# Performance work log

Measured on AMD Instinct MI355X. Metric: run time of the kernel, lower is better.

## Reference

```python
import jax, jax.numpy as jnp
import numpy as np

N_BRANCH, N_LAYER = 4, 3
B, T, D_IN = 4, 1024, 32
D_MODEL, D_INNER, D_STATE, D_CONV, DT_RANK = 128, 256, 16, 4, 8
EMBED = 64
MAX_NORM = 10.0  # safe_expmap0 tangent-norm clip
EPS = 1e-7


def setup_inputs() -> dict:
    key = jax.random.key(0)
    ks = jax.random.split(key, 12)
    def nrm(k, shp, s=0.02):
        return s * jax.random.normal(k, shp, dtype=jnp.float32)
    A_init = jnp.log(jnp.arange(1, D_STATE + 1, dtype=jnp.float32))
    return {
        "trend": jax.random.normal(ks[0], (B, T, D_IN), jnp.float32),
        "seasonal_coarse": jax.random.normal(ks[1], (B, T, D_IN), jnp.float32),
        "seasonal_fine": jax.random.normal(ks[2], (B, T, D_IN), jnp.float32),
        "residual": jax.random.normal(ks[3], (B, T, D_IN), jnp.float32),
        "W_ip": nrm(ks[4], (N_BRANCH, D_IN, D_MODEL)),
        "b_ip": jnp.zeros((N_BRANCH, D_MODEL), jnp.float32),
        "W_in": nrm(ks[5], (N_BRANCH, N_LAYER, D_MODEL, 2 * D_INNER)),
        "conv_w": nrm(ks[6], (N_BRANCH, N_LAYER, D_INNER, D_CONV), 0.1),
        "conv_b": jnp.zeros((N_BRANCH, N_LAYER, D_INNER), jnp.float32),
        "W_x": nrm(ks[7], (N_BRANCH, N_LAYER, D_INNER, DT_RANK + 2 * D_STATE)),
        "W_dt": nrm(ks[8], (N_BRANCH, N_LAYER, DT_RANK, D_INNER), 0.1),
        "b_dt": jnp.full((N_BRANCH, N_LAYER, D_INNER), -4.6, jnp.float32),  # softplus ~ 0.01
        "A_log": jnp.broadcast_to(A_init, (N_BRANCH, N_LAYER, D_INNER, D_STATE)),
        "D_param": jnp.ones((N_BRANCH, N_LAYER, D_INNER), jnp.float32),
        "W_out": nrm(ks[9], (N_BRANCH, N_LAYER, D_INNER, D_MODEL)),
        "W_op": nrm(ks[10], (N_BRANCH, D_MODEL, EMBED)),
        "b_op": jnp.zeros((N_BRANCH, EMBED), jnp.float32),
        "eff_scale": jnp.asarray(0.1, jnp.float32),
    }


def _mamba_layer(x, Win, cw, cb, Wx, Wdt, bdt, Alog, Dp, Wout):
    # x: [B, T, d_model]
    Tlen = x.shape[1]
    xz = x @ Win                                   # [B,T,2*di]
    xp, z = jnp.split(xz, 2, axis=-1)
    # causal depthwise conv1d, kernel D_CONV
    xpad = jnp.pad(xp, ((0, 0), (D_CONV - 1, 0), (0, 0)))
    xc = sum(xpad[:, k:k + Tlen, :] * cw[:, k] for k in range(D_CONV))
    xc = jax.nn.silu(xc + cb)                      # [B,T,di]
    dbl = xc @ Wx                                  # [B,T,r+2s]
    dt = jax.nn.softplus(dbl[..., :DT_RANK] @ Wdt + bdt)   # [B,T,di]
    Bm = dbl[..., DT_RANK:DT_RANK + D_STATE]       # [B,T,s]
    Cm = dbl[..., DT_RANK + D_STATE:]              # [B,T,s]
    A = -jnp.exp(Alog)                             # [di,s]
    dA = jnp.exp(dt[..., None] * A)                # [B,T,di,s]
    dBx = (dt * xc)[..., None] * Bm[:, :, None, :] # [B,T,di,s]

    def step(h, inp):
        dA_t, dBx_t, C_t = inp
        h = dA_t * h + dBx_t
        return h, jnp.einsum('bds,bs->bd', h, C_t)

    h0 = jnp.zeros((x.shape[0], D_INNER, D_STATE), x.dtype)
    _, ys = jax.lax.scan(step, h0, (jnp.swapaxes(dA, 0, 1),
                                     jnp.swapaxes(dBx, 0, 1),
                                     jnp.swapaxes(Cm, 0, 1)))
    y = jnp.swapaxes(ys, 0, 1) + Dp * xc
    return (y * jax.nn.silu(z)) @ Wout


def _embed(x, Wip, bip, Wins, cws, cbs, Wxs, Wdts, bdts, Alogs, Dps, Wouts, Wop, bop):
    h = x @ Wip + bip
    for l in range(N_LAYER):
        h = _mamba_layer(h, Wins[l], cws[l], cbs[l], Wxs[l], Wdts[l], bdts[l],
                         Alogs[l], Dps[l], Wouts[l])
    return h.mean(axis=1) @ Wop + bop              # [B, EMBED]


def _expmap0(v):
    # safe expmap0 on Lorentz (k=1): clip tangent norm at MAX_NORM
    n = jnp.linalg.norm(v, axis=-1, keepdims=True)
    nc = jnp.clip(n, EPS, MAX_NORM)
    v = v * (nc / jnp.maximum(n, EPS))
    return jnp.concatenate([jnp.cosh(nc), jnp.sinh(nc) / nc * v], axis=-1)


def _projx(x):
    sp = x[..., 1:]
    t = jnp.sqrt(1.0 + jnp.sum(sp * sp, axis=-1, keepdims=True))
    return jnp.concatenate([t, sp], axis=-1)


def _logmap0(x):
    sp = x[..., 1:]
    t = jnp.maximum(x[..., :1], 1.0 + EPS)
    d = jnp.arccosh(t)
    spn = jnp.maximum(jnp.linalg.norm(sp, axis=-1, keepdims=True), EPS)
    return d * sp / spn


def _forward(trend, seasonal_coarse, seasonal_fine, residual,
             W_ip, b_ip, W_in, conv_w, conv_b, W_x, W_dt, b_dt,
             A_log, D_param, W_out, W_op, b_op, eff_scale):
    xs = [trend, seasonal_coarse, seasonal_fine, residual]
    z_t = [
        _embed(xs[b], W_ip[b], b_ip[b], W_in[b], conv_w[b], conv_b[b], W_x[b],
               W_dt[b], b_dt[b], A_log[b], D_param[b], W_out[b], W_op[b], b_op[b])
        for b in range(N_BRANCH)
    ]
    es = jnp.tanh(eff_scale)
    z_h = [_projx(_expmap0(z * es)) for z in z_t]
    us = [_logmap0(zh) for zh in z_h]
    combined_tangent = us[0] + us[1] + us[2] + us[3]
    combined_h = _projx(_expmap0(combined_tangent * es))
    return (*z_t, *z_h, combined_tangent, combined_h)


def reference(trend, seasonal_coarse, seasonal_fine, residual,
              W_ip, b_ip, W_in, conv_w, conv_b, W_x, W_dt, b_dt,
              A_log, D_param, W_out, W_op, b_op, eff_scale):
    return _forward(trend, seasonal_coarse, seasonal_fine, residual,
                    W_ip, b_ip, W_in, conv_w, conv_b, W_x, W_dt, b_dt,
                    A_log, D_param, W_out, W_op, b_op, eff_scale)
```

## Files before the change

kernel.cpp:

```cpp
#include <hip/hip_runtime.h>
#include <math.h>

#define NBR 4
#define NLAY 3
#define Bk 4
#define Tk 1024
#define DIN 32
#define DMODEL 128
#define DINNER 256
#define DSTATE 16
#define DTRANK 8
#define EMBEDk 64
#define BT (Bk*Tk)
#define EPSF 1e-7f
#define MAXNF 10.0f
#define LCH 64
#define NCH (Tk/LCH)
#define UF 8
#define NWB 320

typedef __bf16 bf16x8 __attribute__((ext_vector_type(8)));
typedef float  f32x4  __attribute__((ext_vector_type(4)));
typedef unsigned short u16x8 __attribute__((ext_vector_type(8)));

__device__ __forceinline__ float siluf(float x){ return x / (1.f + __expf(-x)); }
__device__ __forceinline__ float softplusf(float x){ return (x > 20.f) ? x : log1pf(__expf(x)); }
__device__ __forceinline__ unsigned short f2b(float x){
    union { float f; unsigned u; } v; v.f = x;
    unsigned r = v.u + 0x7FFF + ((v.u >> 16) & 1);
    return (unsigned short)(r >> 16);
}
__device__ __forceinline__ float b2f(unsigned short u){
    union { unsigned u; float f; } v; v.u = ((unsigned)u) << 16; return v.f;
}

__device__ __forceinline__ void dA_pow(float q, float* dA){
    dA[0] = q;             dA[1] = q * q;
    dA[2] = dA[1] * dA[0]; dA[3] = dA[1] * dA[1];
    dA[4] = dA[3] * dA[0]; dA[5] = dA[3] * dA[1];
    dA[6] = dA[3] * dA[2]; dA[7] = dA[3] * dA[3];
    #pragma unroll
    for (int s = 8; s < 16; ++s) dA[s] = dA[s - 8] * dA[7];
}
__device__ __forceinline__ void dA_exp(float dtv, const float* Aa, float* dA){
    #pragma unroll
    for (int s = 0; s < 16; ++s) dA[s] = __expf(dtv * Aa[s]);
}

template<int MODE>
__global__ __launch_bounds__(256) void bgemm_k(
    const unsigned short* __restrict__ Ab, long aBr, int K,
    const unsigned short* __restrict__ Bt, long bBr,
    float* __restrict__ C0, long c0Br,
    float* __restrict__ C1, long c1Br,
    unsigned short* __restrict__ Cb, long cbBr,
    unsigned short* __restrict__ Cb2, long cb2Br,
    float* __restrict__ Mb,
    const float* __restrict__ bias, long biasBr)
{
    const int br = blockIdx.z;
    Ab += (long)br * aBr;
    Bt += (long)br * bBr;
    if (MODE == 3) { C0 += (long)br * c0Br; C1 += (long)br * c1Br;
                     bias += (long)br * biasBr; }
    if (MODE == 0) { Cb += (long)br * cbBr; Cb2 += (long)br * cb2Br; }
    if (MODE == 1) { Mb += (long)br * (Bk * DMODEL); }
    const int m0 = blockIdx.x * 64, n0 = blockIdx.y * 64;
    __shared__ __align__(16) unsigned short As[8 * 64 * 8];
    __shared__ __align__(16) unsigned short Bs[8 * 64 * 8];
    const int tid = threadIdx.x;
    const int lane = tid & 63, w = tid >> 6;
    const int wm = w >> 1, wn = w & 1;
    const int quad = lane >> 4, l15 = lane & 15;
    f32x4 acc00 = {0,0,0,0}, acc01 = {0,0,0,0}, acc10 = {0,0,0,0}, acc11 = {0,0,0,0};
    for (int kc = 0; kc < K; kc += 64) {
        #pragma unroll
        for (int it = 0; it < 2; ++it) {
            const int c = tid + it * 256;
            const int r = c & 63, kch = c >> 6;
            *(u16x8*)&As[(kch * 64 + r) * 8] =
                *(const u16x8*)(Ab + (long)(m0 + r) * K + kc + kch * 8);
            *(u16x8*)&Bs[(kch * 64 + r) * 8] =
                *(const u16x8*)(Bt + (long)(n0 + r) * K + kc + kch * 8);
        }
        __syncthreads();
        #pragma unroll
        for (int k0 = 0; k0 < 64; k0 += 32) {
            const int kch = (k0 >> 3) + quad;
            bf16x8 a0 = *(const bf16x8*)&As[(kch * 64 + wm * 32 +      l15) * 8];
            bf16x8 a1 = *(const bf16x8*)&As[(kch * 64 + wm * 32 + 16 + l15) * 8];
            bf16x8 b0 = *(const bf16x8*)&Bs[(kch * 64 + wn * 32 +      l15) * 8];
            bf16x8 b1 = *(const bf16x8*)&Bs[(kch * 64 + wn * 32 + 16 + l15) * 8];
            acc00 = __builtin_amdgcn_mfma_f32_16x16x32_bf16(a0, b0, acc00, 0, 0, 0);
            acc01 = __builtin_amdgcn_mfma_f32_16x16x32_bf16(a0, b1, acc01, 0, 0, 0);
            acc10 = __builtin_amdgcn_mfma_f32_16x16x32_bf16(a1, b0, acc10, 0, 0, 0);
            acc11 = __builtin_amdgcn_mfma_f32_16x16x32_bf16(a1, b1, acc11, 0, 0, 0);
        }
        __syncthreads();
    }
    if (MODE == 1) {
        float s0 = 0.f, s1 = 0.f;
        #pragma unroll
        for (int r = 0; r < 4; ++r) { s0 += acc00[r] + acc10[r];
                                      s1 += acc01[r] + acc11[r]; }
        const int bidx = m0 >> 10;
        atomicAdd(&Mb[bidx * DMODEL + n0 + wn * 32 + l15], s0);
        atomicAdd(&Mb[bidx * DMODEL + n0 + wn * 32 + 16 + l15], s1);
        return;
    }
    #pragma unroll
    for (int e = 0; e < 4; ++e) {
        f32x4 a = (e == 0) ? acc00 : (e == 1) ? acc01 : (e == 2) ? acc10 : acc11;
        const int msub = (e >> 1) * 16, nsub = (e & 1) * 16;
        const int col = n0 + wn * 32 + nsub + l15;
        #pragma unroll
        for (int r = 0; r < 4; ++r) {
            const int row = m0 + wm * 32 + msub + quad * 4 + r;
            const float v = a[r];
            if (MODE == 0) {
                if (n0 < 256) Cb[(long)row * 256 + col] = f2b(v);
                else          Cb2[(long)row * 256 + (col - 256)] = f2b(siluf(v));
            } else {
                if (col < 256)      C0[(long)row * 256 + col] = softplusf(v + bias[col]);
                else if (col < 288) C1[(long)row * 32 + (col - 256)] = v;
            }
        }
    }
}

__global__ __launch_bounds__(256) void sgemmW_k(
    const float* __restrict__ Wout, const float* __restrict__ Win,
    float* __restrict__ Wtmp, unsigned* __restrict__ zbuf)
{
    if (blockIdx.x == 0 && blockIdx.y == 0 && blockIdx.z == 0) {
        for (int i = threadIdx.x; i < 4096; i += 256) zbuf[i] = 0u;
    }
    const int z = blockIdx.z, p = z >> 2, br = z & 3;
    const float* A  = Wout + (long)(br * NLAY + p) * DINNER * DMODEL;
    const float* Bw = Win  + (long)(br * NLAY + p + 1) * DMODEL * 512;
    float* C = Wtmp + (long)z * DINNER * 512;
    const int m0 = blockIdx.x * 64, n0 = blockIdx.y * 64;
    __shared__ float As[32][68];
    __shared__ float Bs[32][68];
    const int tid = threadIdx.x;
    const int tx = tid & 15, ty = tid >> 4;
    float acc[4][4] = {};
    for (int kc = 0; kc < DMODEL; kc += 32) {
        #pragma unroll
        for (int it = 0; it < 2; ++it) {
            int id = tid + it * 256;
            int r = id >> 3, c4 = (id & 7) << 2;
            float4 v = *(const float4*)(A + (long)(m0 + r) * DMODEL + kc + c4);
            As[c4+0][r] = v.x; As[c4+1][r] = v.y; As[c4+2][r] = v.z; As[c4+3][r] = v.w;
            int rb = id >> 4, cb = (id & 15) << 2;
            *(float4*)&Bs[rb][cb] = *(const float4*)(Bw + (long)(kc + rb) * 512 + n0 + cb);
        }
        __syncthreads();
        #pragma unroll
        for (int kk = 0; kk < 32; ++kk) {
            float4 a4 = *(const float4*)&As[kk][ty << 2];
            float4 b4 = *(const float4*)&Bs[kk][tx << 2];
            float av[4] = {a4.x, a4.y, a4.z, a4.w};
            float bv[4] = {b4.x, b4.y, b4.z, b4.w};
            #pragma unroll
            for (int i = 0; i < 4; ++i)
                #pragma unroll
                for (int j = 0; j < 4; ++j)
                    acc[i][j] = fmaf(av[i], bv[j], acc[i][j]);
        }
        __syncthreads();
    }
    #pragma unroll
    for (int i = 0; i < 4; ++i) {
        int row = m0 + (ty << 2) + i, col = n0 + (tx << 2);
        float4 v4; v4.x = acc[i][0]; v4.y = acc[i][1]; v4.z = acc[i][2]; v4.w = acc[i][3];
        *(float4*)(C + (long)row * 512 + col) = v4;
    }
}

__device__ void transposeTile(const float* __restrict__ W,
                              unsigned short* __restrict__ o,
                              int Kd, int Nd, int n0, int k0, float* smem)
{
    float (*tile)[65] = (float(*)[65])smem;
    const int t = threadIdx.x;
    #pragma unroll
    for (int i = 0; i < 16; ++i) {
        int idx = t + i * 256;
        int kl = idx >> 6, nl = idx & 63;
        tile[kl][nl] = W[(long)(k0 + kl) * Nd + n0 + nl];
    }
    __syncthreads();
    #pragma unroll
    for (int i = 0; i < 16; ++i) {
        int idx = t + i * 256;
        int nl = idx >> 6, kl = idx & 63;
        o[(long)(n0 + nl) * Kd + k0 + kl] = f2b(tile[kl][nl]);
    }
}

__global__ __launch_bounds__(256) void prepAll_k(
    const float* __restrict__ W_in, const float* __restrict__ Wtmp,
    const float* __restrict__ W_out,
    const float* __restrict__ W_x, const float* __restrict__ W_dt,
    const float* __restrict__ X0, const float* __restrict__ X1,
    const float* __restrict__ X2, const float* __restrict__ X3,
    const float* __restrict__ W_ip, const float* __restrict__ b_ip,
    unsigned short* __restrict__ Win0T, unsigned short* __restrict__ WfT,
    unsigned short* __restrict__ Wo2T, unsigned short* __restrict__ WcT,
    unsigned short* __restrict__ h_bf)
{
    __shared__ float smem[32 * 68 * 2];
    const int id = blockIdx.x;
    if (id < 64) {
        int br = id >> 4, rem = id & 15;
        int nt = rem & 7, kt = rem >> 3;
        transposeTile(W_in + (long)br * NLAY * DMODEL * 512,
                      Win0T + (long)br * 512 * DMODEL,
                      DMODEL, 512, nt * 64, kt * 64, smem);
    } else if (id < 320) {
        int id2 = id - 64;
        int z = id2 >> 5, rem = id2 & 31;
        int nt = rem & 7, kt = rem >> 3;
        transposeTile(Wtmp + (long)z * DINNER * 512,
                      WfT + (long)z * 512 * DINNER,
                      DINNER, 512, nt * 64, kt * 64, smem);
    } else if (id < 352) {
        int id3 = id - 320;
        int br = id3 >> 3, rem = id3 & 7;
        int nt = rem & 1, kt = rem >> 1;
        transposeTile(W_out + ((long)br * NLAY + 2) * DINNER * DMODEL,
                      Wo2T + (long)br * DMODEL * DINNER,
                      DINNER, DMODEL, nt * 64, kt * 64, smem);
    } else if (id < 4192) {
        int id4 = id - 352;
        int bl = id4 / NWB, n = id4 % NWB;
        const int k = threadIdx.x;
        const float* WxP = W_x + (long)bl * DINNER * 40;
        float v;
        if (n < 256) {
            const float* WdtP = W_dt + (long)bl * DTRANK * DINNER;
            float s = 0.f;
            #pragma unroll
            for (int r = 0; r < 8; ++r)
                s = fmaf(WxP[k * 40 + r], WdtP[r * DINNER + n], s);
            v = s;
        } else if (n < 288) {
            v = WxP[k * 40 + 8 + (n - 256)];
        } else {
            v = 0.f;
        }
        WcT[(long)bl * NWB * DINNER + (long)n * DINNER + k] = f2b(v);
    } else {
        int id5 = id - 4192;
        int br = id5 >> 7, rem = id5 & 127;
        int m0 = (rem & 63) * 64, n0 = (rem >> 6) * 64;
        const float* A = (br == 1) ? X1 : (br == 2) ? X2 : (br == 3) ? X3 : X0;
        const float* Bw = W_ip + (long)br * DIN * DMODEL;
        const float* bias = b_ip + (long)br * DMODEL;
        unsigned short* Cb = h_bf + (long)br * BT * DMODEL;
        float (*As)[68] = (float(*)[68])smem;
        float (*Bs)[68] = (float(*)[68])(smem + 32 * 68);
        const int tid = threadIdx.x;
        const int tx = tid & 15, ty = tid >> 4;
        float acc[4][4] = {};
        #pragma unroll
        for (int it = 0; it < 2; ++it) {
            int idd = tid + it * 256;
            int r = idd >> 3, c4 = (idd & 7) << 2;
            float4 v = *(const float4*)(A + (long)(m0 + r) * DIN + c4);
            As[c4+0][r] = v.x; As[c4+1][r] = v.y; As[c4+2][r] = v.z; As[c4+3][r] = v.w;
            int rb = idd >> 4, cb = (idd & 15) << 2;
            *(float4*)&Bs[rb][cb] = *(const float4*)(Bw + (long)rb * DMODEL + n0 + cb);
        }
        __syncthreads();
        #pragma unroll
        for (int kk = 0; kk < 32; ++kk) {
            float4 a4 = *(const float4*)&As[kk][ty << 2];
            float4 b4 = *(const float4*)&Bs[kk][tx << 2];
            float av[4] = {a4.x, a4.y, a4.z, a4.w};
            float bv[4] = {b4.x, b4.y, b4.z, b4.w};
            #pragma unroll
            for (int i = 0; i < 4; ++i)
                #pragma unroll
                for (int j = 0; j < 4; ++j)
                    acc[i][j] = fmaf(av[i], bv[j], acc[i][j]);
        }
        const int col = n0 + (tx << 2);
        #pragma unroll
        for (int i = 0; i < 4; ++i) {
            const int row = m0 + (ty << 2) + i;
            #pragma unroll
            for (int j = 0; j < 4; ++j)
                Cb[(long)row * DMODEL + col + j] = f2b(acc[i][j] + bias[col + j]);
        }
    }
}

__global__ __launch_bounds__(256) void conv_k(
    const unsigned short* __restrict__ xp, const float* __restrict__ cw,
    const float* __restrict__ cb, unsigned short* __restrict__ xcb, int layer)
{
    const int br = blockIdx.y;
    const long base = (long)br * BT * DINNER;
    const int idx = blockIdx.x * 256 + threadIdx.x;
    const int d = idx & (DINNER - 1);
    const int row = idx >> 8;
    const int t = row & (Tk - 1);
    const float4 w4 = *(const float4*)(cw + ((long)(br * NLAY + layer) * DINNER + d) * 4);
    const float wv[4] = {w4.x, w4.y, w4.z, w4.w};
    float acc = cb[(br * NLAY + layer) * DINNER + d];
    const unsigned short* xpb = xp + base + idx;
    #pragma unroll
    for (int k = 0; k < 4; ++k) {
        int tt = t + k - 3;
        if (tt >= 0) acc = fmaf(b2f(xpb[(long)(k - 3) * DINNER]), wv[k], acc);
    }
    xcb[base + idx] = f2b(siluf(acc));
}

__global__ __launch_bounds__(256) void scan1_k(
    const float* __restrict__ dtb, const unsigned short* __restrict__ xcb,
    const float* __restrict__ bcb, const float* __restrict__ Alog,
    float* __restrict__ recbuf, int layer)
{
    const int c = blockIdx.x, b = blockIdx.y, br = blockIdx.z;
    const int d = threadIdx.x;
    const float* Ap = Alog + ((long)(br * NLAY + layer) * DINNER + d) * DSTATE;
    float Aa[16];
    bool pw = true;
    #pragma unroll
    for (int s = 0; s < 16; ++s) {
        Aa[s] = -__expf(Ap[s]);
        pw = pw && (fabsf(Aa[s] + (float)(s + 1)) < 1e-3f);
    }
    const long rbase = (long)br * BT + (long)b * Tk + (long)c * LCH;
    const float* dtp = dtb + rbase * DINNER + d;
    const unsigned short* xcp = xcb + rbase * DINNER + d;
    __shared__ float bcs[LCH * 32];
    {
        const float4* g = (const float4*)(bcb + rbase * 32);
        float4* l = (float4*)bcs;
        l[d] = g[d]; l[d + 256] = g[d + 256];
    }
    float dtc[UF], xcc[UF];
    #pragma unroll
    for (int u = 0; u < UF; ++u) {
        dtc[u] = dtp[(long)u * DINNER];
        xcc[u] = b2f(xcp[(long)u * DINNER]);
    }
    __syncthreads();
    float h[16];
    #pragma unroll
    for (int s = 0; s < 16; ++s) h[s] = 0.f;
    float sumdt = 0.f;
    for (int base = 0; base < LCH; base += UF) {
        const int nb = (base + UF < LCH) ? base + UF : base;
        float dtn[UF], xcn[UF];
        #pragma unroll
        for (int u = 0; u < UF; ++u) {
            dtn[u] = dtp[(long)(nb + u) * DINNER];
            xcn[u] = b2f(xcp[(long)(nb + u) * DINNER]);
        }
        #pragma unroll
        for (int u = 0; u < UF; ++u) {
            const int t = base + u;
            const float dtv = dtc[u];
            const float dtxc = dtv * xcc[u];
            sumdt += dtv;
            float dA[16];
            if (pw) dA_pow(__expf(-dtv), dA);
            else    dA_exp(dtv, Aa, dA);
            const float* bcT = bcs + t * 32;
            #pragma unroll
            for (int s = 0; s < 16; ++s)
                h[s] = fmaf(dA[s], h[s], dtxc * bcT[s]);
        }
        #pragma unroll
        for (int u = 0; u < UF; ++u) { dtc[u] = dtn[u]; xcc[u] = xcn[u]; }
    }
    float* sb = recbuf + (((long)(br * 4 + b) * (NCH - 1) + c) * 17) * 256 + d;
    #pragma unroll
    for (int s = 0; s < 16; ++s) sb[s * 256] = h[s];
    sb[16 * 256] = sumdt;
}

__global__ __launch_bounds__(256) void scan3_k(
    const float* __restrict__ dtb, const unsigned short* __restrict__ xcb,
    const float* __restrict__ bcb, const unsigned short* __restrict__ zb,
    const float* __restrict__ Alog, const float* __restrict__ Dpar,
    const float* __restrict__ recbuf, unsigned short* __restrict__ yzb, int layer)
{
    const int c = blockIdx.x, b = blockIdx.y, br = blockIdx.z;
    const int d = threadIdx.x;
    const float* Ap = Alog + ((long)(br * NLAY + layer) * DINNER + d) * DSTATE;
    float Aa[16];
    bool pw = true;
    #pragma unroll
    for (int s = 0; s < 16; ++s) {
        Aa[s] = -__expf(Ap[s]);
        pw = pw && (fabsf(Aa[s] + (float)(s + 1)) < 1e-3f);
    }
    float h[16];
    #pragma unroll
    for (int s = 0; s < 16; ++s) h[s] = 0.f;
    if (c > 0) {
        const float* recB = recbuf + ((long)(br * 4 + b) * (NCH - 1)) * 17 * 256 + d;
        float rh[16], rs;
        #pragma unroll
        for (int s = 0; s < 16; ++s) rh[s] = recB[s * 256];
        rs = recB[16 * 256];
        for (int cc = 0; cc < c; ++cc) {
            float nh[16], ns = 0.f;
            if (cc + 1 < c) {
                const float* r2 = recB + (long)(cc + 1) * 17 * 256;
                #pragma unroll
                for (int s = 0; s < 16; ++s) nh[s] = r2[s * 256];
                ns = r2[16 * 256];
            } else {
                #pragma unroll
                for (int s = 0; s < 16; ++s) nh[s] = 0.f;
            }
            float P[16];
            if (pw) dA_pow(__expf(-rs), P);
            else    dA_exp(rs, Aa, P);
            #pragma unroll
            for (int s = 0; s < 16; ++s) h[s] = fmaf(h[s], P[s], rh[s]);
            #pragma unroll
            for (int s = 0; s < 16; ++s) rh[s] = nh[s];
            rs = ns;
        }
    }
    const float Dp = Dpar[(br * NLAY + layer) * DINNER + d];
    const long rbase = (long)br * BT + (long)b * Tk + (long)c * LCH;
    const float* dtp = dtb + rbase * DINNER + d;
    const unsigned short* xcp = xcb + rbase * DINNER + d;
    const unsigned short* zp  = zb  + rbase * DINNER + d;
    unsigned short* yp = yzb + rbase * DINNER + d;
    __shared__ float bcs[LCH * 32];
    {
        const float4* g = (const float4*)(bcb + rbase * 32);
        float4* l = (float4*)bcs;
        l[d] = g[d]; l[d + 256] = g[d + 256];
    }
    float dtc[UF], xcc[UF], zc[UF];
    #pragma unroll
    for (int u = 0; u < UF; ++u) {
        dtc[u] = dtp[(long)u * DINNER];
        xcc[u] = b2f(xcp[(long)u * DINNER]);
        zc[u]  = b2f(zp[(long)u * DINNER]);
    }
    __syncthreads();
    for (int base = 0; base < LCH; base += UF) {
        const int nb = (base + UF < LCH) ? base + UF : base;
        float dtn[UF], xcn[UF], zn[UF];
        #pragma unroll
        for (int u = 0; u < UF; ++u) {
            dtn[u] = dtp[(long)(nb + u) * DINNER];
            xcn[u] = b2f(xcp[(long)(nb + u) * DINNER]);
            zn[u]  = b2f(zp[(long)(nb + u) * DINNER]);
        }
        #pragma unroll
        for (int u = 0; u < UF; ++u) {
            const int t = base + u;
            const float dtv = dtc[u], xcv = xcc[u];
            const float dtxc = dtv * xcv;
            float dA[16];
            if (pw) dA_pow(__expf(-dtv), dA);
            else    dA_exp(dtv, Aa, dA);
            const float* bcT = bcs + t * 32;
            #pragma unroll
            for (int s = 0; s < 16; ++s)
                h[s] = fmaf(dA[s], h[s], dtxc * bcT[s]);
            float y0 = 0.f, y1 = 0.f, y2 = 0.f, y3 = 0.f;
            #pragma unroll
            for (int s = 0; s < 16; s += 4) {
                y0 = fmaf(h[s+0], bcT[16+s+0], y0);
                y1 = fmaf(h[s+1], bcT[16+s+1], y1);
                y2 = fmaf(h[s+2], bcT[16+s+2], y2);
                y3 = fmaf(h[s+3], bcT[16+s+3], y3);
            }
            const float y = (y0 + y1) + (y2 + y3) + Dp * xcv;
            yp[(long)t * DINNER] = f2b(y * zc[u]);
        }
        #pragma unroll
        for (int u = 0; u < UF; ++u) { dtc[u] = dtn[u]; xcc[u] = xcn[u]; zc[u] = zn[u]; }
    }
}

__global__ __launch_bounds__(64) void final_k(
    const float* __restrict__ Mb, const float* __restrict__ Wop,
    const float* __restrict__ bop, float* __restrict__ out,
    const float* __restrict__ eff)
{
    __shared__ float hm[NBR * Bk * DMODEL];
    __shared__ float zts[NBR * Bk * EMBEDk];
    __shared__ float us[NBR][Bk][EMBEDk];
    const int t = threadIdx.x;
    for (int i = t; i < NBR * Bk * DMODEL; i += 64) hm[i] = Mb[i] * (1.0f / Tk);
    __syncthreads();
    for (int br = 0; br < NBR; ++br) {
        const float* wp = Wop + (long)br * DMODEL * EMBEDk + t;
        const float bb = bop[br * EMBEDk + t];
        for (int b = 0; b < Bk; ++b) {
            const float* hmp = &hm[(br * Bk + b) * DMODEL];
            float acc = bb;
            for (int k = 0; k < DMODEL; ++k) acc = fmaf(hmp[k], wp[k * EMBEDk], acc);
            out[(br * Bk + b) * EMBEDk + t] = acc;
            zts[(br * Bk + b) * EMBEDk + t] = acc;
        }
    }
    __syncthreads();
    const float es = tanhf(eff[0]);
    if (t < 16) {
        const int br = t >> 2, b = t & 3;
        const float* z = &zts[(br * Bk + b) * EMBEDk];
        float n2 = 0.f;
        for (int e = 0; e < EMBEDk; ++e) { float v = z[e] * es; n2 = fmaf(v, v, n2); }
        const float n  = sqrtf(n2);
        const float nc = fminf(fmaxf(n, EPSF), MAXNF);
        const float sc = nc / fmaxf(n, EPSF);
        const float sh = sinhf(nc) / nc;
        const float fac = es * sc * sh;
        float* zh = out + 1024 + br * (Bk * (EMBEDk + 1)) + b * (EMBEDk + 1);
        float sp2 = 0.f;
        for (int e = 0; e < EMBEDk; ++e) {
            float spv = z[e] * fac;
            sp2 = fmaf(spv, spv, sp2);
            zh[1 + e] = spv;
            us[br][b][e] = spv;
        }
        const float t0 = sqrtf(1.f + sp2);
        zh[0] = t0;
        const float dd  = acoshf(fmaxf(t0, 1.f + EPSF));
        const float spn = fmaxf(sqrtf(sp2), EPSF);
        const float rr  = dd / spn;
        for (int e = 0; e < EMBEDk; ++e) us[br][b][e] *= rr;
    }
    __syncthreads();
    if (t < 4) {
        const int b = t;
        float ct[EMBEDk];
        float* cto = out + 2064 + b * EMBEDk;
        for (int e = 0; e < EMBEDk; ++e) {
            float v = us[0][b][e] + us[1][b][e] + us[2][b][e] + us[3][b][e];
            ct[e] = v; cto[e] = v;
        }
        float n2 = 0.f;
        for (int e = 0; e < EMBEDk; ++e) { float v = ct[e] * es; n2 = fmaf(v, v, n2); }
        const float n  = sqrtf(n2);
        const float nc = fminf(fmaxf(n, EPSF), MAXNF);
        const float sc = nc / fmaxf(n, EPSF);
        const float sh = sinhf(nc) / nc;
        const float fac = es * sc * sh;
        float* ch = out + 2320 + b * (EMBEDk + 1);
        float sp2 = 0.f;
        for (int e = 0; e < EMBEDk; ++e) {
            float spv = ct[e] * fac;
            sp2 = fmaf(spv, spv, sp2);
            ch[1 + e] = spv;
        }
        ch[0] = sqrtf(1.f + sp2);
    }
}

extern "C" void kernel_launch(void* const* d_in, const int* in_sizes, int n_in,
                              void* d_out, int out_size, void* d_ws, size_t ws_size,
                              hipStream_t stream)
{
    const float* X0 = (const float*)d_in[0];
    const float* X1 = (const float*)d_in[1];
    const float* X2 = (const float*)d_in[2];
    const float* X3 = (const float*)d_in[3];
    const float* W_ip   = (const float*)d_in[4];
    const float* b_ip   = (const float*)d_in[5];
    const float* W_in   = (const float*)d_in[6];
    const float* conv_w = (const float*)d_in[7];
    const float* conv_b = (const float*)d_in[8];
    const float* W_x    = (const float*)d_in[9];
    const float* W_dt   = (const float*)d_in[10];
    const float* b_dt   = (const float*)d_in[11];
    const float* A_log  = (const float*)d_in[12];
    const float* D_par  = (const float*)d_in[13];
    const float* W_out  = (const float*)d_in[14];
    const float* W_op   = (const float*)d_in[15];
    const float* b_op   = (const float*)d_in[16];
    const float* eff    = (const float*)d_in[17];
    float* out = (float*)d_out;
    float* ws  = (float*)d_ws;

    float* meanb  = ws + 1024;
    float* buf_dt = ws + 4096;
    float* buf_bc = buf_dt + (long)NBR * BT * DINNER;
    float* recbuf = buf_bc + (long)NBR * BT * 32;
    float* Wtmp   = recbuf + (long)16 * (NCH - 1) * 17 * 256;
    unsigned short* h_bf  = (unsigned short*)(Wtmp + (long)8 * DINNER * 512);
    unsigned short* xp_bf = h_bf  + (long)NBR * BT * DMODEL;
    unsigned short* z_bf  = xp_bf + (long)NBR * BT * DINNER;
    unsigned short* xc_bf = z_bf  + (long)NBR * BT * DINNER;
    unsigned short* yz_bf = xc_bf + (long)NBR * BT * DINNER;
    unsigned short* Win0T = yz_bf + (long)NBR * BT * DINNER;
    unsigned short* WfT   = Win0T + (long)NBR * 512 * DMODEL;
    unsigned short* Wo2T  = WfT   + (long)8 * 512 * DINNER;
    unsigned short* WcT   = Wo2T  + (long)NBR * DMODEL * DINNER;

    sgemmW_k<<<dim3(4, 8, 8), 256, 0, stream>>>(W_out, W_in, Wtmp, (unsigned*)ws);
    prepAll_k<<<4704, 256, 0, stream>>>(
        W_in, Wtmp, W_out, W_x, W_dt, X0, X1, X2, X3, W_ip, b_ip,
        Win0T, WfT, Wo2T, WcT, h_bf);

    for (int l = 0; l < NLAY; ++l) {
        if (l == 0) {
            bgemm_k<0><<<dim3(BT / 64, 8, NBR), 256, 0, stream>>>(
                h_bf, (long)BT * DMODEL, DMODEL, Win0T, (long)512 * DMODEL,
                nullptr, 0, nullptr, 0,
                xp_bf, (long)BT * DINNER, z_bf, (long)BT * DINNER,
                nullptr, nullptr, 0);
        } else {
            bgemm_k<0><<<dim3(BT / 64, 8, NBR), 256, 0, stream>>>(
                yz_bf, (long)BT * DINNER, DINNER,
                WfT + (long)(l - 1) * 4 * 512 * DINNER, (long)512 * DINNER,
                nullptr, 0, nullptr, 0,
                xp_bf, (long)BT * DINNER, z_bf, (long)BT * DINNER,
                nullptr, nullptr, 0);
        }
        conv_k<<<dim3((BT * DINNER) / 256, NBR), 256, 0, stream>>>(
            xp_bf, conv_w, conv_b, xc_bf, l);
        bgemm_k<3><<<dim3(BT / 64, NWB / 64, NBR), 256, 0, stream>>>(
            xc_bf, (long)BT * DINNER, DINNER,
            WcT + (long)l * NWB * DINNER, (long)NLAY * NWB * DINNER,
            buf_dt, (long)BT * DINNER, buf_bc, (long)BT * 32,
            nullptr, 0, nullptr, 0,
            nullptr, b_dt + l * DINNER, (long)NLAY * DINNER);
        scan1_k<<<dim3(NCH - 1, Bk, NBR), 256, 0, stream>>>(
            buf_dt, xc_bf, buf_bc, A_log, recbuf, l);
        scan3_k<<<dim3(NCH, Bk, NBR), 256, 0, stream>>>(
            buf_dt, xc_bf, buf_bc, z_bf, A_log, D_par, recbuf, yz_bf, l);
        if (l == NLAY - 1) {
            bgemm_k<1><<<dim3(BT / 64, DMODEL / 64, NBR), 256, 0, stream>>>(
                yz_bf, (long)BT * DINNER, DINNER,
                Wo2T, (long)DMODEL * DINNER,
                nullptr, 0, nullptr, 0, nullptr, 0, nullptr, 0,
                meanb, nullptr, 0);
        }
    }

    final_k<<<1, 64, 0, stream>>>(meanb, W_op, b_op, out, eff);
}
```

Before: 477.3 us.

## Store dt in bf16, halve scan chunks, widen GEMM K tile, fuse weight prep

```diff
diff --git a/kernel.cpp b/kernel.cpp
--- a/kernel.cpp
+++ b/kernel.cpp
@@ -14,7 +14,7 @@
 #define BT (Bk*Tk)
 #define EPSF 1e-7f
 #define MAXNF 10.0f
-#define LCH 64
+#define LCH 32
 #define NCH (Tk/LCH)
 #define UF 8
 #define NWB 320
@@ -22,6 +22,7 @@
 typedef __bf16 bf16x8 __attribute__((ext_vector_type(8)));
 typedef float  f32x4  __attribute__((ext_vector_type(4)));
 typedef unsigned short u16x8 __attribute__((ext_vector_type(8)));
+typedef unsigned short u16x4 __attribute__((ext_vector_type(4)));
 
 __device__ __forceinline__ float siluf(float x){ return x / (1.f + __expf(-x)); }
 __device__ __forceinline__ float softplusf(float x){ return (x > 20.f) ? x : log1pf(__expf(x)); }
@@ -51,7 +52,6 @@
 __global__ __launch_bounds__(256) void bgemm_k(
     const unsigned short* __restrict__ Ab, long aBr, int K,
     const unsigned short* __restrict__ Bt, long bBr,
-    float* __restrict__ C0, long c0Br,
     float* __restrict__ C1, long c1Br,
     unsigned short* __restrict__ Cb, long cbBr,
     unsigned short* __restrict__ Cb2, long cb2Br,
@@ -61,21 +61,21 @@
     const int br = blockIdx.z;
     Ab += (long)br * aBr;
     Bt += (long)br * bBr;
-    if (MODE == 3) { C0 += (long)br * c0Br; C1 += (long)br * c1Br;
+    if (MODE == 0) { Cb += (long)br * cbBr; Cb2 += (long)br * cb2Br; }
+    if (MODE == 3) { Cb += (long)br * cbBr; C1 += (long)br * c1Br;
                      bias += (long)br * biasBr; }
-    if (MODE == 0) { Cb += (long)br * cbBr; Cb2 += (long)br * cb2Br; }
     if (MODE == 1) { Mb += (long)br * (Bk * DMODEL); }
     const int m0 = blockIdx.x * 64, n0 = blockIdx.y * 64;
-    __shared__ __align__(16) unsigned short As[8 * 64 * 8];
-    __shared__ __align__(16) unsigned short Bs[8 * 64 * 8];
+    __shared__ __align__(16) unsigned short As[16 * 64 * 8];
+    __shared__ __align__(16) unsigned short Bs[16 * 64 * 8];
     const int tid = threadIdx.x;
     const int lane = tid & 63, w = tid >> 6;
     const int wm = w >> 1, wn = w & 1;
     const int quad = lane >> 4, l15 = lane & 15;
     f32x4 acc00 = {0,0,0,0}, acc01 = {0,0,0,0}, acc10 = {0,0,0,0}, acc11 = {0,0,0,0};
-    for (int kc = 0; kc < K; kc += 64) {
-        #pragma unroll
-        for (int it = 0; it < 2; ++it) {
+    for (int kc = 0; kc < K; kc += 128) {
+        #pragma unroll
+        for (int it = 0; it < 4; ++it) {
             const int c = tid + it * 256;
             const int r = c & 63, kch = c >> 6;
             *(u16x8*)&As[(kch * 64 + r) * 8] =
@@ -85,7 +85,7 @@
         }
         __syncthreads();
         #pragma unroll
-        for (int k0 = 0; k0 < 64; k0 += 32) {
+        for (int k0 = 0; k0 < 128; k0 += 32) {
             const int kch = (k0 >> 3) + quad;
             bf16x8 a0 = *(const bf16x8*)&As[(kch * 64 + wm * 32 +      l15) * 8];
             bf16x8 a1 = *(const bf16x8*)&As[(kch * 64 + wm * 32 + 16 + l15) * 8];
@@ -121,60 +121,10 @@
                 if (n0 < 256) Cb[(long)row * 256 + col] = f2b(v);
                 else          Cb2[(long)row * 256 + (col - 256)] = f2b(siluf(v));
             } else {
-                if (col < 256)      C0[(long)row * 256 + col] = softplusf(v + bias[col]);
+                if (col < 256)      Cb[(long)row * 256 + col] = f2b(softplusf(v + bias[col]));
                 else if (col < 288) C1[(long)row * 32 + (col - 256)] = v;
             }
         }
-    }
-}
-
-__global__ __launch_bounds__(256) void sgemmW_k(
-    const float* __restrict__ Wout, const float* __restrict__ Win,
-    float* __restrict__ Wtmp, unsigned* __restrict__ zbuf)
-{
-    if (blockIdx.x == 0 && blockIdx.y == 0 && blockIdx.z == 0) {
-        for (int i = threadIdx.x; i < 4096; i += 256) zbuf[i] = 0u;
-    }
-    const int z = blockIdx.z, p = z >> 2, br = z & 3;
-    const float* A  = Wout + (long)(br * NLAY + p) * DINNER * DMODEL;
-    const float* Bw = Win  + (long)(br * NLAY + p + 1) * DMODEL * 512;
-    float* C = Wtmp + (long)z * DINNER * 512;
-    const int m0 = blockIdx.x * 64, n0 = blockIdx.y * 64;
-    __shared__ float As[32][68];
-    __shared__ float Bs[32][68];
-    const int tid = threadIdx.x;
-    const int tx = tid & 15, ty = tid >> 4;
-    float acc[4][4] = {};
-    for (int kc = 0; kc < DMODEL; kc += 32) {
-        #pragma unroll
-        for (int it = 0; it < 2; ++it) {
-            int id = tid + it * 256;
-            int r = id >> 3, c4 = (id & 7) << 2;
-            float4 v = *(const float4*)(A + (long)(m0 + r) * DMODEL + kc + c4);
-            As[c4+0][r] = v.x; As[c4+1][r] = v.y; As[c4+2][r] = v.z; As[c4+3][r] = v.w;
-            int rb = id >> 4, cb = (id & 15) << 2;
-            *(float4*)&Bs[rb][cb] = *(const float4*)(Bw + (long)(kc + rb) * 512 + n0 + cb);
-        }
-        __syncthreads();
-        #pragma unroll
-        for (int kk = 0; kk < 32; ++kk) {
-            float4 a4 = *(const float4*)&As[kk][ty << 2];
-            float4 b4 = *(const float4*)&Bs[kk][tx << 2];
-            float av[4] = {a4.x, a4.y, a4.z, a4.w};
-            float bv[4] = {b4.x, b4.y, b4.z, b4.w};
-            #pragma unroll
-            for (int i = 0; i < 4; ++i)
-                #pragma unroll
-                for (int j = 0; j < 4; ++j)
-                    acc[i][j] = fmaf(av[i], bv[j], acc[i][j]);
-        }
-        __syncthreads();
-    }
-    #pragma unroll
-    for (int i = 0; i < 4; ++i) {
-        int row = m0 + (ty << 2) + i, col = n0 + (tx << 2);
-        float4 v4; v4.x = acc[i][0]; v4.y = acc[i][1]; v4.z = acc[i][2]; v4.w = acc[i][3];
-        *(float4*)(C + (long)row * 512 + col) = v4;
     }
 }
 
@@ -199,16 +149,15 @@
     }
 }
 
-__global__ __launch_bounds__(256) void prepAll_k(
-    const float* __restrict__ W_in, const float* __restrict__ Wtmp,
-    const float* __restrict__ W_out,
+__global__ __launch_bounds__(256) void prep_k(
+    const float* __restrict__ W_in, const float* __restrict__ W_out,
     const float* __restrict__ W_x, const float* __restrict__ W_dt,
     const float* __restrict__ X0, const float* __restrict__ X1,
     const float* __restrict__ X2, const float* __restrict__ X3,
     const float* __restrict__ W_ip, const float* __restrict__ b_ip,
-    unsigned short* __restrict__ Win0T, unsigned short* __restrict__ WfT,
-    unsigned short* __restrict__ Wo2T, unsigned short* __restrict__ WcT,
-    unsigned short* __restrict__ h_bf)
+    unsigned short* __restrict__ Win0T, unsigned short* __restrict__ Wo2T,
+    unsigned short* __restrict__ WcT, unsigned short* __restrict__ h_bf,
+    unsigned short* __restrict__ WfT, unsigned* __restrict__ zbuf)
 {
     __shared__ float smem[32 * 68 * 2];
     const int id = blockIdx.x;
@@ -218,22 +167,15 @@
         transposeTile(W_in + (long)br * NLAY * DMODEL * 512,
                       Win0T + (long)br * 512 * DMODEL,
                       DMODEL, 512, nt * 64, kt * 64, smem);
-    } else if (id < 320) {
-        int id2 = id - 64;
-        int z = id2 >> 5, rem = id2 & 31;
-        int nt = rem & 7, kt = rem >> 3;
-        transposeTile(Wtmp + (long)z * DINNER * 512,
-                      WfT + (long)z * 512 * DINNER,
-                      DINNER, 512, nt * 64, kt * 64, smem);
-    } else if (id < 352) {
-        int id3 = id - 320;
+    } else if (id < 96) {
+        int id3 = id - 64;
         int br = id3 >> 3, rem = id3 & 7;
         int nt = rem & 1, kt = rem >> 1;
         transposeTile(W_out + ((long)br * NLAY + 2) * DINNER * DMODEL,
                       Wo2T + (long)br * DMODEL * DINNER,
                       DINNER, DMODEL, nt * 64, kt * 64, smem);
-    } else if (id < 4192) {
-        int id4 = id - 352;
+    } else if (id < 3936) {
+        int id4 = id - 96;
         int bl = id4 / NWB, n = id4 % NWB;
         const int k = threadIdx.x;
         const float* WxP = W_x + (long)bl * DINNER * 40;
@@ -251,8 +193,8 @@
             v = 0.f;
         }
         WcT[(long)bl * NWB * DINNER + (long)n * DINNER + k] = f2b(v);
-    } else {
-        int id5 = id - 4192;
+    } else if (id < 4448) {
+        int id5 = id - 3936;
         int br = id5 >> 7, rem = id5 & 127;
         int m0 = (rem & 63) * 64, n0 = (rem >> 6) * 64;
         const float* A = (br == 1) ? X1 : (br == 2) ? X2 : (br == 3) ? X3 : X0;
@@ -294,6 +236,57 @@
             for (int j = 0; j < 4; ++j)
                 Cb[(long)row * DMODEL + col + j] = f2b(acc[i][j] + bias[col + j]);
         }
+    } else {
+        if (id == 4448) {
+            for (int i = threadIdx.x; i < 4096; i += 256) zbuf[i] = 0u;
+        }
+        int sid = id - 4448;
+        int z = sid >> 5, rem = sid & 31;
+        int mt = rem >> 3, nt = rem & 7;
+        const int p = z >> 2, br = z & 3;
+        const float* A  = W_out + (long)(br * NLAY + p) * DINNER * DMODEL;
+        const float* Bw = W_in  + (long)(br * NLAY + p + 1) * DMODEL * 512;
+        unsigned short* WfTz = WfT + (long)z * 512 * DINNER;
+        const int m0 = mt * 64, n0 = nt * 64;
+        float (*As)[68] = (float(*)[68])smem;
+        float (*Bs)[68] = (float(*)[68])(smem + 32 * 68);
+        const int tid = threadIdx.x;
+        const int tx = tid & 15, ty = tid >> 4;
+        float acc[4][4] = {};
+        for (int kc = 0; kc < DMODEL; kc += 32) {
+            #pragma unroll
+            for (int it = 0; it < 2; ++it) {
+                int idd = tid + it * 256;
+                int r = idd >> 3, c4 = (idd & 7) << 2;
+                float4 v = *(const float4*)(A + (long)(m0 + r) * DMODEL + kc + c4);
+                As[c4+0][r] = v.x; As[c4+1][r] = v.y; As[c4+2][r] = v.z; As[c4+3][r] = v.w;
+                int rb = idd >> 4, cb = (idd & 15) << 2;
+                *(float4*)&Bs[rb][cb] = *(const float4*)(Bw + (long)(kc + rb) * 512 + n0 + cb);
+            }
+            __syncthreads();
+            #pragma unroll
+            for (int kk = 0; kk < 32; ++kk) {
+                float4 a4 = *(const float4*)&As[kk][ty << 2];
+                float4 b4 = *(const float4*)&Bs[kk][tx << 2];
+                float av[4] = {a4.x, a4.y, a4.z, a4.w};
+                float bv[4] = {b4.x, b4.y, b4.z, b4.w};
+                #pragma unroll
+                for (int i = 0; i < 4; ++i)
+                    #pragma unroll
+                    for (int j = 0; j < 4; ++j)
+                        acc[i][j] = fmaf(av[i], bv[j], acc[i][j]);
+            }
+            __syncthreads();
+        }
+        const int row0 = m0 + (ty << 2);
+        const int col0 = n0 + (tx << 2);
+        #pragma unroll
+        for (int j = 0; j < 4; ++j) {
+            u16x4 t4;
+            #pragma unroll
+            for (int i = 0; i < 4; ++i) t4[i] = f2b(acc[i][j]);
+            *(u16x4*)&WfTz[(long)(col0 + j) * DINNER + row0] = t4;
+        }
     }
 }
 
@@ -320,7 +313,7 @@
 }
 
 __global__ __launch_bounds__(256) void scan1_k(
-    const float* __restrict__ dtb, const unsigned short* __restrict__ xcb,
+    const unsigned short* __restrict__ dtb, const unsigned short* __restrict__ xcb,
     const float* __restrict__ bcb, const float* __restrict__ Alog,
     float* __restrict__ recbuf, int layer)
 {
@@ -335,18 +328,17 @@
         pw = pw && (fabsf(Aa[s] + (float)(s + 1)) < 1e-3f);
     }
     const long rbase = (long)br * BT + (long)b * Tk + (long)c * LCH;
-    const float* dtp = dtb + rbase * DINNER + d;
+    const unsigned short* dtp = dtb + rbase * DINNER + d;
     const unsigned short* xcp = xcb + rbase * DINNER + d;
     __shared__ float bcs[LCH * 32];
     {
         const float4* g = (const float4*)(bcb + rbase * 32);
-        float4* l = (float4*)bcs;
-        l[d] = g[d]; l[d + 256] = g[d + 256];
+        ((float4*)bcs)[d] = g[d];
     }
     float dtc[UF], xcc[UF];
     #pragma unroll
     for (int u = 0; u < UF; ++u) {
-        dtc[u] = dtp[(long)u * DINNER];
+        dtc[u] = b2f(dtp[(long)u * DINNER]);
         xcc[u] = b2f(xcp[(long)u * DINNER]);
     }
     __syncthreads();
@@ -359,7 +351,7 @@
         float dtn[UF], xcn[UF];
         #pragma unroll
         for (int u = 0; u < UF; ++u) {
-            dtn[u] = dtp[(long)(nb + u) * DINNER];
+            dtn[u] = b2f(dtp[(long)(nb + u) * DINNER]);
             xcn[u] = b2f(xcp[(long)(nb + u) * DINNER]);
         }
         #pragma unroll
@@ -386,7 +378,7 @@
 }
 
 __global__ __launch_bounds__(256) void scan3_k(
-    const float* __restrict__ dtb, const unsigned short* __restrict__ xcb,
+    const unsigned short* __restrict__ dtb, const unsigned short* __restrict__ xcb,
     const float* __restrict__ bcb, const unsigned short* __restrict__ zb,
     const float* __restrict__ Alog, const float* __restrict__ Dpar,
     const float* __restrict__ recbuf, unsigned short* __restrict__ yzb, int layer)
@@ -433,20 +425,19 @@
     }
     const float Dp = Dpar[(br * NLAY + layer) * DINNER + d];
     const long rbase = (long)br * BT + (long)b * Tk + (long)c * LCH;
-    const float* dtp = dtb + rbase * DINNER + d;
+    const unsigned short* dtp = dtb + rbase * DINNER + d;
     const unsigned short* xcp = xcb + rbase * DINNER + d;
     const unsigned short* zp  = zb  + rbase * DINNER + d;
     unsigned short* yp = yzb + rbase * DINNER + d;
     __shared__ float bcs[LCH * 32];
     {
         const float4* g = (const float4*)(bcb + rbase * 32);
-        float4* l = (float4*)bcs;
-        l[d] = g[d]; l[d + 256] = g[d + 256];
+        ((float4*)bcs)[d] = g[d];
     }
     float dtc[UF], xcc[UF], zc[UF];
     #pragma unroll
     for (int u = 0; u < UF; ++u) {
-        dtc[u] = dtp[(long)u * DINNER];
+        dtc[u] = b2f(dtp[(long)u * DINNER]);
         xcc[u] = b2f(xcp[(long)u * DINNER]);
         zc[u]  = b2f(zp[(long)u * DINNER]);
     }
@@ -456,7 +447,7 @@
         float dtn[UF], xcn[UF], zn[UF];
         #pragma unroll
         for (int u = 0; u < UF; ++u) {
-            dtn[u] = dtp[(long)(nb + u) * DINNER];
+            dtn[u] = b2f(dtp[(long)(nb + u) * DINNER]);
             xcn[u] = b2f(xcp[(long)(nb + u) * DINNER]);
             zn[u]  = b2f(zp[(long)(nb + u) * DINNER]);
         }
@@ -590,11 +581,10 @@
     float* ws  = (float*)d_ws;
 
     float* meanb  = ws + 1024;
-    float* buf_dt = ws + 4096;
-    float* buf_bc = buf_dt + (long)NBR * BT * DINNER;
+    float* buf_bc = ws + 4096;
     float* recbuf = buf_bc + (long)NBR * BT * 32;
-    float* Wtmp   = recbuf + (long)16 * (NCH - 1) * 17 * 256;
-    unsigned short* h_bf  = (unsigned short*)(Wtmp + (long)8 * DINNER * 512);
+    unsigned short* dt_bf = (unsigned short*)(recbuf + (long)16 * (NCH - 1) * 17 * 256);
+    unsigned short* h_bf  = dt_bf + (long)NBR * BT * DINNER;
     unsigned short* xp_bf = h_bf  + (long)NBR * BT * DMODEL;
     unsigned short* z_bf  = xp_bf + (long)NBR * BT * DINNER;
     unsigned short* xc_bf = z_bf  + (long)NBR * BT * DINNER;
@@ -604,23 +594,22 @@
     unsigned short* Wo2T  = WfT   + (long)8 * 512 * DINNER;
     unsigned short* WcT   = Wo2T  + (long)NBR * DMODEL * DINNER;
 
-    sgemmW_k<<<dim3(4, 8, 8), 256, 0, stream>>>(W_out, W_in, Wtmp, (unsigned*)ws);
-    prepAll_k<<<4704, 256, 0, stream>>>(
-        W_in, Wtmp, W_out, W_x, W_dt, X0, X1, X2, X3, W_ip, b_ip,
-        Win0T, WfT, Wo2T, WcT, h_bf);
+    prep_k<<<4704, 256, 0, stream>>>(
+        W_in, W_out, W_x, W_dt, X0, X1, X2, X3, W_ip, b_ip,
+        Win0T, Wo2T, WcT, h_bf, WfT, (unsigned*)ws);
 
     for (int l = 0; l < NLAY; ++l) {
         if (l == 0) {
             bgemm_k<0><<<dim3(BT / 64, 8, NBR), 256, 0, stream>>>(
                 h_bf, (long)BT * DMODEL, DMODEL, Win0T, (long)512 * DMODEL,
-                nullptr, 0, nullptr, 0,
+                nullptr, 0,
                 xp_bf, (long)BT * DINNER, z_bf, (long)BT * DINNER,
                 nullptr, nullptr, 0);
         } else {
             bgemm_k<0><<<dim3(BT / 64, 8, NBR), 256, 0, stream>>>(
                 yz_bf, (long)BT * DINNER, DINNER,
                 WfT + (long)(l - 1) * 4 * 512 * DINNER, (long)512 * DINNER,
-                nullptr, 0, nullptr, 0,
+                nullptr, 0,
                 xp_bf, (long)BT * DINNER, z_bf, (long)BT * DINNER,
                 nullptr, nullptr, 0);
         }
@@ -629,18 +618,18 @@
         bgemm_k<3><<<dim3(BT / 64, NWB / 64, NBR), 256, 0, stream>>>(
             xc_bf, (long)BT * DINNER, DINNER,
             WcT + (long)l * NWB * DINNER, (long)NLAY * NWB * DINNER,
-            buf_dt, (long)BT * DINNER, buf_bc, (long)BT * 32,
-            nullptr, 0, nullptr, 0,
+            buf_bc, (long)BT * 32,
+            dt_bf, (long)BT * DINNER, nullptr, 0,
             nullptr, b_dt + l * DINNER, (long)NLAY * DINNER);
         scan1_k<<<dim3(NCH - 1, Bk, NBR), 256, 0, stream>>>(
-            buf_dt, xc_bf, buf_bc, A_log, recbuf, l);
+            dt_bf, xc_bf, buf_bc, A_log, recbuf, l);
         scan3_k<<<dim3(NCH, Bk, NBR), 256, 0, stream>>>(
-            buf_dt, xc_bf, buf_bc, z_bf, A_log, D_par, recbuf, yz_bf, l);
+            dt_bf, xc_bf, buf_bc, z_bf, A_log, D_par, recbuf, yz_bf, l);
         if (l == NLAY - 1) {
             bgemm_k<1><<<dim3(BT / 64, DMODEL / 64, NBR), 256, 0, stream>>>(
                 yz_bf, (long)BT * DINNER, DINNER,
                 Wo2T, (long)DMODEL * DINNER,
-                nullptr, 0, nullptr, 0, nullptr, 0, nullptr, 0,
+                nullptr, 0, nullptr, 0, nullptr, 0,
                 meanb, nullptr, 0);
         }
     }
```

Result: no change. 482.0 us (+1.0%).
